# Kernel tuning notes

Hardware: AMD Instinct MI355X
Metric: run time of the kernel (lower is better)

## Reference

```python
import jax, jax.numpy as jnp
import numpy as np

N_NODES = 50000


def setup_inputs() -> dict:
    key = jax.random.key(0)
    k1, k2, k3, k4, k5 = jax.random.split(key, 5)
    x = jax.random.normal(k1, (50000, 256), dtype=jnp.float32)
    edge_rows = jax.random.randint(k2, (1600000,), 0, N_NODES, dtype=jnp.int32)
    edge_cols = jax.random.randint(k3, (1600000,), 0, N_NODES, dtype=jnp.int32)
    edge_vals = jax.random.uniform(k4, (1600000,), dtype=jnp.float32)
    W = jax.random.normal(k5, (256, 128), dtype=jnp.float32) * (6.0 / (256 + 128)) ** 0.5  # glorot scale
    b = jnp.zeros((128,), dtype=jnp.float32)
    return {"x": x, "edge_rows": edge_rows, "edge_cols": edge_cols,
            "edge_vals": edge_vals, "W": W, "b": b}


def reference(x, edge_rows, edge_cols, edge_vals, W, b):
    # pre_sup = x @ W   -> [N, output_dim]
    pre_sup = jnp.matmul(x, W)
    # SpMM: output[r] = sum_{edges e with row r} val_e * pre_sup[col_e]
    msgs = edge_vals[:, None] * pre_sup[edge_cols]          # [E, output_dim]
    output = jax.ops.segment_sum(msgs, edge_rows, num_segments=N_NODES)
    output = output + b
    return jax.nn.relu(output)
```

## Files before the change

kernel.cpp:

```cpp
#include <hip/hip_runtime.h>

#define K_DIM 256
#define OD 128
#define BSH 5
#define BROWS 32
#define BCAP 2048
#define FILL_THREADS 1024
#define FILL_CHUNK 4096
#define NB_MAX 2048

typedef __attribute__((ext_vector_type(8))) short short8;
typedef __attribute__((ext_vector_type(4))) float f32x4;

__device__ inline unsigned short f2bf(float f) {
    unsigned u = __float_as_uint(f);
    unsigned r = (u + 0x7fffu + ((u >> 16) & 1u)) >> 16;
    return (unsigned short)r;
}

union Frag8 { short8 s; uint4 u; };

__global__ __launch_bounds__(256) void init_pack(const float* __restrict__ W,
                                                 uint4* __restrict__ wb,
                                                 int* __restrict__ gcur, int NB) {
    if ((int)blockIdx.x == 16) {
        for (int i = threadIdx.x; i < NB; i += 256) gcur[i * 16] = i * BCAP;
        return;
    }
    int t = blockIdx.x * 256 + threadIdx.x;
    if (t >= 8 * 8 * 64) return;
    int l  = t & 63;
    int n  = (t >> 6) & 7;
    int ks = t >> 9;
    int g  = l >> 4;
    int col = 16 * n + (l & 15);
    int kb  = 32 * ks + 4 * g;
    unsigned short e[8];
    #pragma unroll
    for (int j = 0; j < 8; ++j) {
        int k = kb + (j & 3) + 16 * (j >> 2);
        e[j] = f2bf(W[(size_t)k * OD + col]);
    }
    uint4 u;
    u.x = (unsigned)e[0] | ((unsigned)e[1] << 16);
    u.y = (unsigned)e[2] | ((unsigned)e[3] << 16);
    u.z = (unsigned)e[4] | ((unsigned)e[5] << 16);
    u.w = (unsigned)e[6] | ((unsigned)e[7] << 16);
    wb[t] = u;
}

__global__ __launch_bounds__(256) void gemm_mfma(const float* __restrict__ x,
                                                 const uint4* __restrict__ wb,
                                                 unsigned* __restrict__ prebp, int M) {
    const int t = threadIdx.x;
    const int l = t & 63;
    const int w = t >> 6;
    const int g = l >> 4;
    const int row  = blockIdx.x * 64 + w * 16 + (l & 15);
    const int rowc = row < M ? row : M - 1;
    const float* xp = x + (size_t)rowc * K_DIM + g * 4;

    f32x4 acc[8];
    #pragma unroll
    for (int n = 0; n < 8; ++n) acc[n] = (f32x4){0.f, 0.f, 0.f, 0.f};

    #pragma unroll
    for (int ks = 0; ks < 8; ++ks) {
        float4 xa = *reinterpret_cast<const float4*>(xp + 32 * ks);
        float4 xb = *reinterpret_cast<const float4*>(xp + 32 * ks + 16);
        Frag8 a;
        a.u.x = (unsigned)f2bf(xa.x) | ((unsigned)f2bf(xa.y) << 16);
        a.u.y = (unsigned)f2bf(xa.z) | ((unsigned)f2bf(xa.w) << 16);
        a.u.z = (unsigned)f2bf(xb.x) | ((unsigned)f2bf(xb.y) << 16);
        a.u.w = (unsigned)f2bf(xb.z) | ((unsigned)f2bf(xb.w) << 16);
        const uint4* wp = wb + (size_t)ks * 8 * 64 + l;
        #pragma unroll
        for (int n = 0; n < 8; ++n) {
            Frag8 bfrag;
            bfrag.u = wp[n * 64];
            acc[n] = __builtin_amdgcn_mfma_f32_16x16x32_bf16(a.s, bfrag.s, acc[n], 0, 0, 0);
        }
    }
    const int rbase = blockIdx.x * 64 + w * 16 + g * 4;
    #pragma unroll
    for (int r = 0; r < 4; ++r) {
        int ro = rbase + r;
        if (ro < M) {
            unsigned* dst = prebp + (size_t)ro * 64 + (l & 15);
            #pragma unroll
            for (int m = 0; m < 4; ++m)
                dst[16 * m] = (unsigned)f2bf(acc[m][r]) |
                              ((unsigned)f2bf(acc[m + 4][r]) << 16);
        }
    }
}

__global__ __launch_bounds__(1024) void fill_bucket(const int* __restrict__ rows,
                                                    const int* __restrict__ cols,
                                                    const float* __restrict__ vals,
                                                    int* __restrict__ gcur,
                                                    uint2* __restrict__ csr, int E, int NB) {
    __shared__ int cnt[NB_MAX];
    __shared__ int base[NB_MAX];
    const int t  = threadIdx.x;
    const int e0 = blockIdx.x * FILL_CHUNK;
    for (int i = t; i < NB; i += FILL_THREADS) cnt[i] = 0;
    __syncthreads();
    int  r[4]; int c[4]; float v[4]; bool ok[4];
    #pragma unroll
    for (int it = 0; it < 4; ++it) {
        int i = e0 + it * FILL_THREADS + t;
        ok[it] = (i < E);
        if (ok[it]) {
            r[it] = rows[i];
            c[it] = cols[i];
            v[it] = vals[i];
            atomicAdd(&cnt[r[it] >> BSH], 1);
        }
    }
    __syncthreads();
    for (int bkt = t; bkt < NB; bkt += FILL_THREADS) {
        int cn = cnt[bkt];
        base[bkt] = cn ? atomicAdd(&gcur[bkt * 16], cn) : 0;
    }
    __syncthreads();
    #pragma unroll
    for (int it = 0; it < 4; ++it) {
        if (ok[it]) {
            int pos = atomicAdd(&base[r[it] >> BSH], 1);
            csr[pos] = make_uint2(((unsigned)(r[it] & (BROWS - 1)) << 16) | (unsigned)c[it],
                                  __float_as_uint(v[it]));
        }
    }
}

__global__ __launch_bounds__(256) void gather_sort(const int* __restrict__ gcur,
                                                   const uint2* __restrict__ csr,
                                                   const unsigned* __restrict__ prebp,
                                                   const float* __restrict__ b,
                                                   float* __restrict__ out, int M) {
    __shared__ uint2 sbuf[BCAP];
    __shared__ int cnt[BROWS];
    __shared__ int beg[BROWS];
    __shared__ int ofs[BROWS];
    const int t   = threadIdx.x;
    const int bkt = (int)blockIdx.x;
    const int nE  = gcur[bkt * 16] - bkt * BCAP;
    const uint2* ep = csr + (size_t)bkt * BCAP;

    if (t < BROWS) cnt[t] = 0;
    __syncthreads();
    for (int i = t; i < nE; i += 256)
        atomicAdd(&cnt[ep[i].x >> 16], 1);
    __syncthreads();
    if (t < 64) {
        int c  = (t < BROWS) ? cnt[t] : 0;
        int sc = c;
        #pragma unroll
        for (int o = 1; o < 32; o <<= 1) {
            int u = __shfl_up(sc, o, 64);
            if ((t & 63) >= o) sc += u;
        }
        if (t < BROWS) { beg[t] = sc - c; ofs[t] = sc - c; }
    }
    __syncthreads();
    for (int i = t; i < nE; i += 256) {
        uint2 e = ep[i];
        int r   = (int)(e.x >> 16);
        int pos = atomicAdd(&ofs[r], 1);
        sbuf[pos] = make_uint2(e.x & 0xffffu, e.y);
    }
    __syncthreads();

    const int l = t & 63, w = t >> 6;
    const float bv0 = b[l], bv1 = b[64 + l];
    #pragma unroll 1
    for (int rr = w * 8; rr < w * 8 + 8; ++rr) {
        int r = (bkt << BSH) + rr;
        if (r >= M) continue;
        int j  = beg[rr];
        int je = j + cnt[rr];
        float a0 = 0.f, a1 = 0.f;
        for (; j + 3 < je; j += 4) {
            uint2 e0 = sbuf[j], e1 = sbuf[j + 1], e2 = sbuf[j + 2], e3 = sbuf[j + 3];
            unsigned p0 = prebp[(size_t)e0.x * 64 + l];
            unsigned p1 = prebp[(size_t)e1.x * 64 + l];
            unsigned p2 = prebp[(size_t)e2.x * 64 + l];
            unsigned p3 = prebp[(size_t)e3.x * 64 + l];
            float v0 = __uint_as_float(e0.y), v1 = __uint_as_float(e1.y);
            float v2 = __uint_as_float(e2.y), v3 = __uint_as_float(e3.y);
            a0 = fmaf(v0, __uint_as_float(p0 << 16), a0);
            a1 = fmaf(v0, __uint_as_float(p0 & 0xffff0000u), a1);
            a0 = fmaf(v1, __uint_as_float(p1 << 16), a0);
            a1 = fmaf(v1, __uint_as_float(p1 & 0xffff0000u), a1);
            a0 = fmaf(v2, __uint_as_float(p2 << 16), a0);
            a1 = fmaf(v2, __uint_as_float(p2 & 0xffff0000u), a1);
            a0 = fmaf(v3, __uint_as_float(p3 << 16), a0);
            a1 = fmaf(v3, __uint_as_float(p3 & 0xffff0000u), a1);
        }
        for (; j < je; ++j) {
            uint2 e = sbuf[j];
            unsigned p = prebp[(size_t)e.x * 64 + l];
            float v = __uint_as_float(e.y);
            a0 = fmaf(v, __uint_as_float(p << 16), a0);
            a1 = fmaf(v, __uint_as_float(p & 0xffff0000u), a1);
        }
        out[(size_t)r * OD + l]      = fmaxf(a0 + bv0, 0.f);
        out[(size_t)r * OD + 64 + l] = fmaxf(a1 + bv1, 0.f);
    }
}

__global__ __launch_bounds__(256) void spmm_scatter(const int* __restrict__ rows,
                                                    const int* __restrict__ cols,
                                                    const float* __restrict__ vals,
                                                    const unsigned* __restrict__ prebp,
                                                    float* __restrict__ out, int E) {
    const int e    = (int)((blockIdx.x * 256u + threadIdx.x) >> 6);
    const int lane = threadIdx.x & 63;
    if (e >= E) return;
    const int   r = rows[e];
    const int   c = cols[e];
    const float v = vals[e];
    unsigned p = prebp[(size_t)c * 64 + lane];
    float* o = out + (size_t)r * OD;
    unsafeAtomicAdd(o + lane,      v * __uint_as_float(p << 16));
    unsafeAtomicAdd(o + lane + 64, v * __uint_as_float(p & 0xffff0000u));
}

__global__ __launch_bounds__(256) void bias_relu(float* __restrict__ out,
                                                 const float* __restrict__ b, int n4) {
    int i = blockIdx.x * 256 + threadIdx.x;
    if (i >= n4) return;
    float4 v = reinterpret_cast<float4*>(out)[i];
    int c = (i & ((OD / 4) - 1)) << 2;
    float4 bv = *reinterpret_cast<const float4*>(b + c);
    v.x = fmaxf(v.x + bv.x, 0.f);
    v.y = fmaxf(v.y + bv.y, 0.f);
    v.z = fmaxf(v.z + bv.z, 0.f);
    v.w = fmaxf(v.w + bv.w, 0.f);
    reinterpret_cast<float4*>(out)[i] = v;
}

extern "C" void kernel_launch(void* const* d_in, const int* in_sizes, int n_in,
                              void* d_out, int out_size, void* d_ws, size_t ws_size,
                              hipStream_t stream) {
    const float* x     = (const float*)d_in[0];
    const int*   erows = (const int*)d_in[1];
    const int*   ecols = (const int*)d_in[2];
    const float* evals = (const float*)d_in[3];
    const float* W     = (const float*)d_in[4];
    const float* b     = (const float*)d_in[5];
    float*       out   = (float*)d_out;

    const int M  = in_sizes[0] / K_DIM;
    const int E  = in_sizes[1];
    const int NB = (M + BROWS - 1) >> BSH;

    char* ws = (char*)d_ws;
    size_t off = 0;
    auto alloc = [&](size_t bytes) { char* p = ws + off; off = (off + bytes + 15) & ~(size_t)15; return p; };
    unsigned* prebp = (unsigned*)alloc((size_t)M * 64 * sizeof(unsigned));
    uint4*    wb    = (uint4*)alloc((size_t)8 * 8 * 64 * sizeof(uint4));
    int*      gcur  = (int*)  alloc((size_t)NB * 16 * sizeof(int));
    uint2*    csr   = (uint2*)alloc((size_t)NB * BCAP * sizeof(uint2));
    const bool bucket_ok = (off <= ws_size) && (NB <= NB_MAX) && (M <= 65536);

    const int nGemm = (M + 63) / 64;

    if (bucket_ok) {
        init_pack<<<17, 256, 0, stream>>>(W, wb, gcur, NB);
        gemm_mfma<<<nGemm, 256, 0, stream>>>(x, wb, prebp, M);
        fill_bucket<<<(E + FILL_CHUNK - 1) / FILL_CHUNK, FILL_THREADS, 0, stream>>>(
            erows, ecols, evals, gcur, csr, E, NB);
        gather_sort<<<NB, 256, 0, stream>>>(gcur, csr, prebp, b, out, M);
    } else {
        init_pack<<<16, 256, 0, stream>>>(W, wb, gcur, 0);
        gemm_mfma<<<nGemm, 256, 0, stream>>>(x, wb, prebp, M);
        hipMemsetAsync(d_out, 0, (size_t)out_size * sizeof(float), stream);
        spmm_scatter<<<(E + 3) / 4, 256, 0, stream>>>(erows, ecols, evals, prebp, out, E);
        bias_relu<<<(out_size / 4 + 255) / 256, 256, 0, stream>>>(out, b, out_size / 4);
    }
}
```

Baseline: 123.3 us.

## Fuse GEMM and edge bucketing into one launch, widen gather blocks

Merges the MFMA GEMM and the edge bucket fill into a single kernel launch, with separate blocks doing each job, so the two independent stages can run concurrently and one launch is saved. The block size grows to 512 for both the fused kernel and the gather kernel. In the gather kernel the edges are now held in registers between the count and scatter passes, so they are read from global memory once, and the gather loop is unrolled to 8 outstanding loads. The fused kernel reserves shared memory for the fill path even in GEMM blocks, which may lower occupancy. The gather also now clamps the bucket count to BCAP.

```diff
diff --git a/kernel.cpp b/kernel.cpp
--- a/kernel.cpp
+++ b/kernel.cpp
@@ -5,7 +5,6 @@
 #define BSH 5
 #define BROWS 32
 #define BCAP 2048
-#define FILL_THREADS 1024
 #define FILL_CHUNK 4096
 #define NB_MAX 2048
 
@@ -49,14 +48,53 @@
     wb[t] = u;
 }
 
-__global__ __launch_bounds__(256) void gemm_mfma(const float* __restrict__ x,
+__global__ __launch_bounds__(512) void gemm_fill(const float* __restrict__ x,
                                                  const uint4* __restrict__ wb,
-                                                 unsigned* __restrict__ prebp, int M) {
+                                                 unsigned* __restrict__ prebp,
+                                                 const int* __restrict__ rows,
+                                                 const int* __restrict__ cols,
+                                                 const float* __restrict__ vals,
+                                                 int* __restrict__ gcur,
+                                                 uint2* __restrict__ csr,
+                                                 int M, int E, int NB, int nGemm) {
+    __shared__ int cnt[NB_MAX];
+    __shared__ int base[NB_MAX];
     const int t = threadIdx.x;
+
+    if ((int)blockIdx.x >= nGemm) {
+        const int e0 = ((int)blockIdx.x - nGemm) * FILL_CHUNK;
+        for (int i = t; i < NB; i += 512) cnt[i] = 0;
+        __syncthreads();
+        int r[8]; int c[8]; float v[8];
+        #pragma unroll
+        for (int it = 0; it < 8; ++it) {
+            int i = e0 + it * 512 + t;
+            if (i < E) {
+                r[it] = rows[i]; c[it] = cols[i]; v[it] = vals[i];
+                atomicAdd(&cnt[r[it] >> BSH], 1);
+            } else r[it] = -1;
+        }
+        __syncthreads();
+        for (int bkt = t; bkt < NB; bkt += 512) {
+            int cn = cnt[bkt];
+            base[bkt] = cn ? atomicAdd(&gcur[bkt * 16], cn) : 0;
+        }
+        __syncthreads();
+        #pragma unroll
+        for (int it = 0; it < 8; ++it) {
+            if (r[it] >= 0) {
+                int pos = atomicAdd(&base[r[it] >> BSH], 1);
+                csr[pos] = make_uint2(((unsigned)(r[it] & (BROWS - 1)) << 16) | (unsigned)c[it],
+                                      __float_as_uint(v[it]));
+            }
+        }
+        return;
+    }
+
     const int l = t & 63;
     const int w = t >> 6;
     const int g = l >> 4;
-    const int row  = blockIdx.x * 64 + w * 16 + (l & 15);
+    const int row  = blockIdx.x * 128 + w * 16 + (l & 15);
     const int rowc = row < M ? row : M - 1;
     const float* xp = x + (size_t)rowc * K_DIM + g * 4;
 
@@ -81,7 +119,7 @@
             acc[n] = __builtin_amdgcn_mfma_f32_16x16x32_bf16(a.s, bfrag.s, acc[n], 0, 0, 0);
         }
     }
-    const int rbase = blockIdx.x * 64 + w * 16 + g * 4;
+    const int rbase = blockIdx.x * 128 + w * 16 + g * 4;
     #pragma unroll
     for (int r = 0; r < 4; ++r) {
         int ro = rbase + r;
@@ -95,46 +133,7 @@
     }
 }
 
-__global__ __launch_bounds__(1024) void fill_bucket(const int* __restrict__ rows,
-                                                    const int* __restrict__ cols,
-                                                    const float* __restrict__ vals,
-                                                    int* __restrict__ gcur,
-                                                    uint2* __restrict__ csr, int E, int NB) {
-    __shared__ int cnt[NB_MAX];
-    __shared__ int base[NB_MAX];
-    const int t  = threadIdx.x;
-    const int e0 = blockIdx.x * FILL_CHUNK;
-    for (int i = t; i < NB; i += FILL_THREADS) cnt[i] = 0;
-    __syncthreads();
-    int  r[4]; int c[4]; float v[4]; bool ok[4];
-    #pragma unroll
-    for (int it = 0; it < 4; ++it) {
-        int i = e0 + it * FILL_THREADS + t;
-        ok[it] = (i < E);
-        if (ok[it]) {
-            r[it] = rows[i];
-            c[it] = cols[i];
-            v[it] = vals[i];
-            atomicAdd(&cnt[r[it] >> BSH], 1);
-        }
-    }
-    __syncthreads();
-    for (int bkt = t; bkt < NB; bkt += FILL_THREADS) {
-        int cn = cnt[bkt];
-        base[bkt] = cn ? atomicAdd(&gcur[bkt * 16], cn) : 0;
-    }
-    __syncthreads();
-    #pragma unroll
-    for (int it = 0; it < 4; ++it) {
-        if (ok[it]) {
-            int pos = atomicAdd(&base[r[it] >> BSH], 1);
-            csr[pos] = make_uint2(((unsigned)(r[it] & (BROWS - 1)) << 16) | (unsigned)c[it],
-                                  __float_as_uint(v[it]));
-        }
-    }
-}
-
-__global__ __launch_bounds__(256) void gather_sort(const int* __restrict__ gcur,
+__global__ __launch_bounds__(512) void gather_sort(const int* __restrict__ gcur,
                                                    const uint2* __restrict__ csr,
                                                    const unsigned* __restrict__ prebp,
                                                    const float* __restrict__ b,
@@ -145,13 +144,21 @@
     __shared__ int ofs[BROWS];
     const int t   = threadIdx.x;
     const int bkt = (int)blockIdx.x;
-    const int nE  = gcur[bkt * 16] - bkt * BCAP;
+    int nE = gcur[bkt * 16] - bkt * BCAP;
+    nE = nE < BCAP ? nE : BCAP;
     const uint2* ep = csr + (size_t)bkt * BCAP;
 
     if (t < BROWS) cnt[t] = 0;
     __syncthreads();
-    for (int i = t; i < nE; i += 256)
-        atomicAdd(&cnt[ep[i].x >> 16], 1);
+    uint2 er[4];
+    #pragma unroll
+    for (int k = 0; k < 4; ++k) {
+        int i = t + k * 512;
+        if (i < nE) {
+            er[k] = ep[i];
+            atomicAdd(&cnt[er[k].x >> 16], 1);
+        } else er[k].x = 0xffffffffu;
+    }
     __syncthreads();
     if (t < 64) {
         int c  = (t < BROWS) ? cnt[t] : 0;
@@ -164,31 +171,42 @@
         if (t < BROWS) { beg[t] = sc - c; ofs[t] = sc - c; }
     }
     __syncthreads();
-    for (int i = t; i < nE; i += 256) {
-        uint2 e = ep[i];
-        int r   = (int)(e.x >> 16);
-        int pos = atomicAdd(&ofs[r], 1);
-        sbuf[pos] = make_uint2(e.x & 0xffffu, e.y);
+    #pragma unroll
+    for (int k = 0; k < 4; ++k) {
+        if (er[k].x != 0xffffffffu) {
+            int r   = (int)(er[k].x >> 16);
+            int pos = atomicAdd(&ofs[r], 1);
+            sbuf[pos] = make_uint2(er[k].x & 0xffffu, er[k].y);
+        }
     }
     __syncthreads();
 
     const int l = t & 63, w = t >> 6;
     const float bv0 = b[l], bv1 = b[64 + l];
+    const unsigned* pl = prebp + l;
     #pragma unroll 1
-    for (int rr = w * 8; rr < w * 8 + 8; ++rr) {
-        int r = (bkt << BSH) + rr;
+    for (int q = 0; q < 4; ++q) {
+        int rr = w + 8 * q;
+        int r  = (bkt << BSH) + rr;
         if (r >= M) continue;
         int j  = beg[rr];
         int je = j + cnt[rr];
         float a0 = 0.f, a1 = 0.f;
-        for (; j + 3 < je; j += 4) {
-            uint2 e0 = sbuf[j], e1 = sbuf[j + 1], e2 = sbuf[j + 2], e3 = sbuf[j + 3];
-            unsigned p0 = prebp[(size_t)e0.x * 64 + l];
-            unsigned p1 = prebp[(size_t)e1.x * 64 + l];
-            unsigned p2 = prebp[(size_t)e2.x * 64 + l];
-            unsigned p3 = prebp[(size_t)e3.x * 64 + l];
+        for (; j + 7 < je; j += 8) {
+            uint2 e0 = sbuf[j],     e1 = sbuf[j + 1], e2 = sbuf[j + 2], e3 = sbuf[j + 3];
+            uint2 e4 = sbuf[j + 4], e5 = sbuf[j + 5], e6 = sbuf[j + 6], e7 = sbuf[j + 7];
+            unsigned p0 = pl[(size_t)e0.x * 64];
+            unsigned p1 = pl[(size_t)e1.x * 64];
+            unsigned p2 = pl[(size_t)e2.x * 64];
+            unsigned p3 = pl[(size_t)e3.x * 64];
+            unsigned p4 = pl[(size_t)e4.x * 64];
+            unsigned p5 = pl[(size_t)e5.x * 64];
+            unsigned p6 = pl[(size_t)e6.x * 64];
+            unsigned p7 = pl[(size_t)e7.x * 64];
             float v0 = __uint_as_float(e0.y), v1 = __uint_as_float(e1.y);
             float v2 = __uint_as_float(e2.y), v3 = __uint_as_float(e3.y);
+            float v4 = __uint_as_float(e4.y), v5 = __uint_as_float(e5.y);
+            float v6 = __uint_as_float(e6.y), v7 = __uint_as_float(e7.y);
             a0 = fmaf(v0, __uint_as_float(p0 << 16), a0);
             a1 = fmaf(v0, __uint_as_float(p0 & 0xffff0000u), a1);
             a0 = fmaf(v1, __uint_as_float(p1 << 16), a0);
@@ -197,10 +215,18 @@
             a1 = fmaf(v2, __uint_as_float(p2 & 0xffff0000u), a1);
             a0 = fmaf(v3, __uint_as_float(p3 << 16), a0);
             a1 = fmaf(v3, __uint_as_float(p3 & 0xffff0000u), a1);
+            a0 = fmaf(v4, __uint_as_float(p4 << 16), a0);
+            a1 = fmaf(v4, __uint_as_float(p4 & 0xffff0000u), a1);
+            a0 = fmaf(v5, __uint_as_float(p5 << 16), a0);
+            a1 = fmaf(v5, __uint_as_float(p5 & 0xffff0000u), a1);
+            a0 = fmaf(v6, __uint_as_float(p6 << 16), a0);
+            a1 = fmaf(v6, __uint_as_float(p6 & 0xffff0000u), a1);
+            a0 = fmaf(v7, __uint_as_float(p7 << 16), a0);
+            a1 = fmaf(v7, __uint_as_float(p7 & 0xffff0000u), a1);
         }
         for (; j < je; ++j) {
             uint2 e = sbuf[j];
-            unsigned p = prebp[(size_t)e.x * 64 + l];
+            unsigned p = pl[(size_t)e.x * 64];
             float v = __uint_as_float(e.y);
             a0 = fmaf(v, __uint_as_float(p << 16), a0);
             a1 = fmaf(v, __uint_as_float(p & 0xffff0000u), a1);
@@ -265,17 +291,18 @@
     uint2*    csr   = (uint2*)alloc((size_t)NB * BCAP * sizeof(uint2));
     const bool bucket_ok = (off <= ws_size) && (NB <= NB_MAX) && (M <= 65536);
 
-    const int nGemm = (M + 63) / 64;
+    const int nGemm = (M + 127) / 128;
+    const int nFill = (E + FILL_CHUNK - 1) / FILL_CHUNK;
 
     if (bucket_ok) {
         init_pack<<<17, 256, 0, stream>>>(W, wb, gcur, NB);
-        gemm_mfma<<<nGemm, 256, 0, stream>>>(x, wb, prebp, M);
-        fill_bucket<<<(E + FILL_CHUNK - 1) / FILL_CHUNK, FILL_THREADS, 0, stream>>>(
-            erows, ecols, evals, gcur, csr, E, NB);
-        gather_sort<<<NB, 256, 0, stream>>>(gcur, csr, prebp, b, out, M);
+        gemm_fill<<<nGemm + nFill, 512, 0, stream>>>(x, wb, prebp, erows, ecols, evals,
+                                                     gcur, csr, M, E, NB, nGemm);
+        gather_sort<<<NB, 512, 0, stream>>>(gcur, csr, prebp, b, out, M);
     } else {
         init_pack<<<16, 256, 0, stream>>>(W, wb, gcur, 0);
-        gemm_mfma<<<nGemm, 256, 0, stream>>>(x, wb, prebp, M);
+        gemm_fill<<<nGemm, 512, 0, stream>>>(x, wb, prebp, nullptr, nullptr, nullptr,
+                                             nullptr, nullptr, M, 0, 0, nGemm);
         hipMemsetAsync(d_out, 0, (size_t)out_size * sizeof(float), stream);
         spmm_scatter<<<(E + 3) / 4, 256, 0, stream>>>(erows, ecols, evals, prebp, out, E);
         bias_relu<<<(out_size / 4 + 255) / 256, 256, 0, stream>>>(out, b, out_size / 4);
```

New measurement: 119.6 us. 1.03x faster.

## Split pre-support into column quarters and compress edge records for gather

Applied to the files above, without the earlier changes.

The pre-support matrix is stored as four column-quarter planes. Each gather block now handles one quarter of the output columns for a bucket, with 16-lane groups working on separate edges and a shuffle reduction at the end. Edge records shrink from 8 bytes to 4 (column index plus bf16 value) with a separate 1-byte row array, and edges stay in registers between the count and scatter passes. The quarter planes are meant to make each block's gathered working set smaller so it stays in cache, at the cost of four times as many blocks, each re-reading and re-sorting its bucket, and of bf16 rounding on the edge values.

```diff
diff --git a/kernel.cpp b/kernel.cpp
--- a/kernel.cpp
+++ b/kernel.cpp
@@ -86,11 +86,10 @@
     for (int r = 0; r < 4; ++r) {
         int ro = rbase + r;
         if (ro < M) {
-            unsigned* dst = prebp + (size_t)ro * 64 + (l & 15);
             #pragma unroll
             for (int m = 0; m < 4; ++m)
-                dst[16 * m] = (unsigned)f2bf(acc[m][r]) |
-                              ((unsigned)f2bf(acc[m + 4][r]) << 16);
+                prebp[((size_t)m * M + ro) * 16 + (l & 15)] =
+                    (unsigned)f2bf(acc[m][r]) | ((unsigned)f2bf(acc[m + 4][r]) << 16);
         }
     }
 }
@@ -99,7 +98,9 @@
                                                     const int* __restrict__ cols,
                                                     const float* __restrict__ vals,
                                                     int* __restrict__ gcur,
-                                                    uint2* __restrict__ csr, int E, int NB) {
+                                                    unsigned* __restrict__ csr32,
+                                                    unsigned char* __restrict__ crow,
+                                                    int E, int NB) {
     __shared__ int cnt[NB_MAX];
     __shared__ int base[NB_MAX];
     const int t  = threadIdx.x;
@@ -128,30 +129,46 @@
     for (int it = 0; it < 4; ++it) {
         if (ok[it]) {
             int pos = atomicAdd(&base[r[it] >> BSH], 1);
-            csr[pos] = make_uint2(((unsigned)(r[it] & (BROWS - 1)) << 16) | (unsigned)c[it],
-                                  __float_as_uint(v[it]));
-        }
-    }
-}
-
-__global__ __launch_bounds__(256) void gather_sort(const int* __restrict__ gcur,
-                                                   const uint2* __restrict__ csr,
-                                                   const unsigned* __restrict__ prebp,
-                                                   const float* __restrict__ b,
-                                                   float* __restrict__ out, int M) {
-    __shared__ uint2 sbuf[BCAP];
+            csr32[pos] = ((unsigned)c[it] << 16) | (unsigned)f2bf(v[it]);
+            crow[pos]  = (unsigned char)(r[it] & (BROWS - 1));
+        }
+    }
+}
+
+__global__ __launch_bounds__(256) void gather_q(const int* __restrict__ gcur,
+                                                const unsigned* __restrict__ csr32,
+                                                const unsigned char* __restrict__ crow,
+                                                const unsigned* __restrict__ prebp,
+                                                const float* __restrict__ b,
+                                                float* __restrict__ out,
+                                                int M, int NB, int KHALF) {
+    __shared__ unsigned sbuf[BCAP];
     __shared__ int cnt[BROWS];
     __shared__ int beg[BROWS];
     __shared__ int ofs[BROWS];
-    const int t   = threadIdx.x;
-    const int bkt = (int)blockIdx.x;
-    const int nE  = gcur[bkt * 16] - bkt * BCAP;
-    const uint2* ep = csr + (size_t)bkt * BCAP;
+    const int slot = (int)blockIdx.x & 7;
+    const int kk   = (int)blockIdx.x >> 3;
+    const int q    = slot >> 1;
+    const int bkt  = kk + (slot & 1) * KHALF;
+    if (bkt >= NB) return;
+    const int t = threadIdx.x;
+    int nE = gcur[bkt * 16] - bkt * BCAP;
+    nE = nE < BCAP ? nE : BCAP;
+    const unsigned*      ce = csr32 + (size_t)bkt * BCAP;
+    const unsigned char* re = crow  + (size_t)bkt * BCAP;
 
     if (t < BROWS) cnt[t] = 0;
     __syncthreads();
-    for (int i = t; i < nE; i += 256)
-        atomicAdd(&cnt[ep[i].x >> 16], 1);
+    unsigned er[8]; int rw[8];
+    #pragma unroll
+    for (int k2 = 0; k2 < 8; ++k2) {
+        int i = t + k2 * 256;
+        if (i < nE) {
+            er[k2] = __builtin_nontemporal_load(ce + i);
+            rw[k2] = (int)__builtin_nontemporal_load(re + i);
+            atomicAdd(&cnt[rw[k2]], 1);
+        } else rw[k2] = -1;
+    }
     __syncthreads();
     if (t < 64) {
         int c  = (t < BROWS) ? cnt[t] : 0;
@@ -164,49 +181,56 @@
         if (t < BROWS) { beg[t] = sc - c; ofs[t] = sc - c; }
     }
     __syncthreads();
-    for (int i = t; i < nE; i += 256) {
-        uint2 e = ep[i];
-        int r   = (int)(e.x >> 16);
-        int pos = atomicAdd(&ofs[r], 1);
-        sbuf[pos] = make_uint2(e.x & 0xffffu, e.y);
+    #pragma unroll
+    for (int k2 = 0; k2 < 8; ++k2) {
+        if (rw[k2] >= 0) {
+            int pos = atomicAdd(&ofs[rw[k2]], 1);
+            sbuf[pos] = er[k2];
+        }
     }
     __syncthreads();
 
     const int l = t & 63, w = t >> 6;
-    const float bv0 = b[l], bv1 = b[64 + l];
+    const int g16 = l >> 4, l16 = l & 15;
+    const unsigned* qbase = prebp + ((size_t)q * M) * 16 + l16;
+    const float bv0 = b[q * 16 + l16];
+    const float bv1 = b[q * 16 + l16 + 64];
     #pragma unroll 1
-    for (int rr = w * 8; rr < w * 8 + 8; ++rr) {
-        int r = (bkt << BSH) + rr;
+    for (int r8 = 0; r8 < 8; ++r8) {
+        const int rr = w + 4 * r8;
+        const int r  = (bkt << BSH) + rr;
         if (r >= M) continue;
         int j  = beg[rr];
         int je = j + cnt[rr];
         float a0 = 0.f, a1 = 0.f;
-        for (; j + 3 < je; j += 4) {
-            uint2 e0 = sbuf[j], e1 = sbuf[j + 1], e2 = sbuf[j + 2], e3 = sbuf[j + 3];
-            unsigned p0 = prebp[(size_t)e0.x * 64 + l];
-            unsigned p1 = prebp[(size_t)e1.x * 64 + l];
-            unsigned p2 = prebp[(size_t)e2.x * 64 + l];
-            unsigned p3 = prebp[(size_t)e3.x * 64 + l];
-            float v0 = __uint_as_float(e0.y), v1 = __uint_as_float(e1.y);
-            float v2 = __uint_as_float(e2.y), v3 = __uint_as_float(e3.y);
-            a0 = fmaf(v0, __uint_as_float(p0 << 16), a0);
-            a1 = fmaf(v0, __uint_as_float(p0 & 0xffff0000u), a1);
-            a0 = fmaf(v1, __uint_as_float(p1 << 16), a0);
-            a1 = fmaf(v1, __uint_as_float(p1 & 0xffff0000u), a1);
-            a0 = fmaf(v2, __uint_as_float(p2 << 16), a0);
-            a1 = fmaf(v2, __uint_as_float(p2 & 0xffff0000u), a1);
-            a0 = fmaf(v3, __uint_as_float(p3 << 16), a0);
-            a1 = fmaf(v3, __uint_as_float(p3 & 0xffff0000u), a1);
-        }
-        for (; j < je; ++j) {
-            uint2 e = sbuf[j];
-            unsigned p = prebp[(size_t)e.x * 64 + l];
-            float v = __uint_as_float(e.y);
+        for (; j + 8 <= je; j += 8) {
+            unsigned eA = sbuf[j + g16];
+            unsigned eB = sbuf[j + 4 + g16];
+            unsigned pA = qbase[(size_t)(eA >> 16) * 16];
+            unsigned pB = qbase[(size_t)(eB >> 16) * 16];
+            float vA = __uint_as_float(eA << 16);
+            float vB = __uint_as_float(eB << 16);
+            a0 = fmaf(vA, __uint_as_float(pA << 16), a0);
+            a1 = fmaf(vA, __uint_as_float(pA & 0xffff0000u), a1);
+            a0 = fmaf(vB, __uint_as_float(pB << 16), a0);
+            a1 = fmaf(vB, __uint_as_float(pB & 0xffff0000u), a1);
+        }
+        for (; j < je; j += 4) {
+            int idx = j + g16;
+            unsigned e = (idx < je) ? sbuf[idx] : 0u;
+            unsigned p = qbase[(size_t)(e >> 16) * 16];
+            float v = __uint_as_float(e << 16);
             a0 = fmaf(v, __uint_as_float(p << 16), a0);
             a1 = fmaf(v, __uint_as_float(p & 0xffff0000u), a1);
         }
-        out[(size_t)r * OD + l]      = fmaxf(a0 + bv0, 0.f);
-        out[(size_t)r * OD + 64 + l] = fmaxf(a1 + bv1, 0.f);
+        a0 += __shfl_xor(a0, 16, 64); a0 += __shfl_xor(a0, 32, 64);
+        a1 += __shfl_xor(a1, 16, 64); a1 += __shfl_xor(a1, 32, 64);
+        if (g16 == 0) {
+            __builtin_nontemporal_store(fmaxf(a0 + bv0, 0.f),
+                                        out + (size_t)r * OD + q * 16 + l16);
+            __builtin_nontemporal_store(fmaxf(a1 + bv1, 0.f),
+                                        out + (size_t)r * OD + q * 16 + l16 + 64);
+        }
     }
 }
 
@@ -214,17 +238,18 @@
                                                     const int* __restrict__ cols,
                                                     const float* __restrict__ vals,
                                                     const unsigned* __restrict__ prebp,
-                                                    float* __restrict__ out, int E) {
+                                                    float* __restrict__ out, int E, int M) {
     const int e    = (int)((blockIdx.x * 256u + threadIdx.x) >> 6);
     const int lane = threadIdx.x & 63;
     if (e >= E) return;
     const int   r = rows[e];
     const int   c = cols[e];
     const float v = vals[e];
-    unsigned p = prebp[(size_t)c * 64 + lane];
+    const int m = lane >> 4, l16 = lane & 15;
+    unsigned p = prebp[((size_t)m * M + c) * 16 + l16];
     float* o = out + (size_t)r * OD;
-    unsafeAtomicAdd(o + lane,      v * __uint_as_float(p << 16));
-    unsafeAtomicAdd(o + lane + 64, v * __uint_as_float(p & 0xffff0000u));
+    unsafeAtomicAdd(o + 16 * m + l16,      v * __uint_as_float(p << 16));
+    unsafeAtomicAdd(o + 16 * m + l16 + 64, v * __uint_as_float(p & 0xffff0000u));
 }
 
 __global__ __launch_bounds__(256) void bias_relu(float* __restrict__ out,
@@ -255,14 +280,16 @@
     const int M  = in_sizes[0] / K_DIM;
     const int E  = in_sizes[1];
     const int NB = (M + BROWS - 1) >> BSH;
+    const int KHALF = (NB + 1) / 2;
 
     char* ws = (char*)d_ws;
     size_t off = 0;
     auto alloc = [&](size_t bytes) { char* p = ws + off; off = (off + bytes + 15) & ~(size_t)15; return p; };
-    unsigned* prebp = (unsigned*)alloc((size_t)M * 64 * sizeof(unsigned));
-    uint4*    wb    = (uint4*)alloc((size_t)8 * 8 * 64 * sizeof(uint4));
-    int*      gcur  = (int*)  alloc((size_t)NB * 16 * sizeof(int));
-    uint2*    csr   = (uint2*)alloc((size_t)NB * BCAP * sizeof(uint2));
+    unsigned*      prebp = (unsigned*)alloc((size_t)M * 64 * sizeof(unsigned));
+    uint4*         wb    = (uint4*)alloc((size_t)8 * 8 * 64 * sizeof(uint4));
+    int*           gcur  = (int*)  alloc((size_t)NB * 16 * sizeof(int));
+    unsigned*      csr32 = (unsigned*)alloc((size_t)NB * BCAP * sizeof(unsigned));
+    unsigned char* crow  = (unsigned char*)alloc((size_t)NB * BCAP);
     const bool bucket_ok = (off <= ws_size) && (NB <= NB_MAX) && (M <= 65536);
 
     const int nGemm = (M + 63) / 64;
@@ -271,13 +298,14 @@
         init_pack<<<17, 256, 0, stream>>>(W, wb, gcur, NB);
         gemm_mfma<<<nGemm, 256, 0, stream>>>(x, wb, prebp, M);
         fill_bucket<<<(E + FILL_CHUNK - 1) / FILL_CHUNK, FILL_THREADS, 0, stream>>>(
-            erows, ecols, evals, gcur, csr, E, NB);
-        gather_sort<<<NB, 256, 0, stream>>>(gcur, csr, prebp, b, out, M);
+            erows, ecols, evals, gcur, csr32, crow, E, NB);
+        gather_q<<<8 * KHALF, 256, 0, stream>>>(gcur, csr32, crow, prebp, b, out,
+                                                M, NB, KHALF);
     } else {
         init_pack<<<16, 256, 0, stream>>>(W, wb, gcur, 0);
         gemm_mfma<<<nGemm, 256, 0, stream>>>(x, wb, prebp, M);
         hipMemsetAsync(d_out, 0, (size_t)out_size * sizeof(float), stream);
-        spmm_scatter<<<(E + 3) / 4, 256, 0, stream>>>(erows, ecols, evals, prebp, out, E);
+        spmm_scatter<<<(E + 3) / 4, 256, 0, stream>>>(erows, ecols, evals, prebp, out, E, M);
         bias_relu<<<(out_size / 4 + 255) / 256, 256, 0, stream>>>(out, b, out_size / 4);
     }
 }
```

New measurement: 144.9 us. 1.18x slower.
